# Kernel tuning notes

Hardware: AMD Instinct MI355X
Metric: run time of the kernel (lower is better)

## Reference

```python
import jax, jax.numpy as jnp
import numpy as np

B, H, S_AX, NH, STEPS = 64, 1024, 16384, 8, 16
DH = H // NH
SCALE = 1.0 / np.sqrt(DH)


def setup_inputs():
    key = jax.random.key(0)
    ks = jax.random.split(key, 16)
    s = 0.02
    w = lambda k, shp: jax.random.normal(k, shp, jnp.float32) * s
    return {
        'conjecture': jax.random.normal(ks[0], (B, H), jnp.float32),
        'axiom_emb': jax.random.normal(ks[1], (S_AX, H), jnp.float32),
        'ax_in_w': w(ks[2], (3 * H, H)), 'ax_in_b': jnp.zeros((3 * H,), jnp.float32),
        'ax_out_w': w(ks[3], (H, H)), 'ax_out_b': jnp.zeros((H,), jnp.float32),
        'st_in_w': w(ks[4], (3 * H, H)), 'st_in_b': jnp.zeros((3 * H,), jnp.float32),
        'st_out_w': w(ks[5], (H, H)), 'st_out_b': jnp.zeros((H,), jnp.float32),
        'gen_w1': w(ks[6], (2 * H, 3 * H)), 'gen_b1': jnp.zeros((2 * H,), jnp.float32),
        'ln_g': jnp.ones((2 * H,), jnp.float32), 'ln_b': jnp.zeros((2 * H,), jnp.float32),
        'gen_w2': w(ks[7], (H, 2 * H)), 'gen_b2': jnp.zeros((H,), jnp.float32),
        'val_w1': w(ks[8], (H, H)), 'val_b1': jnp.zeros((H,), jnp.float32),
        'val_w2': w(ks[9], (1, H)), 'val_b2': jnp.zeros((1,), jnp.float32),
        'wih0': w(ks[10], (4 * H, H)), 'whh0': w(ks[11], (4 * H, H)),
        'bih0': jnp.zeros((4 * H,), jnp.float32), 'bhh0': jnp.zeros((4 * H,), jnp.float32),
        'wih1': w(ks[12], (4 * H, H)), 'whh1': w(ks[13], (4 * H, H)),
        'bih1': jnp.zeros((4 * H,), jnp.float32), 'bhh1': jnp.zeros((4 * H,), jnp.float32),
        'max_steps': STEPS,
    }


def _layernorm(x, g, b, eps=1e-5):
    m = x.mean(-1, keepdims=True)
    v = jnp.mean((x - m) ** 2, axis=-1, keepdims=True)
    return (x - m) / jnp.sqrt(v + eps) * g + b


def _lstm_cell(x, h, c, wih, whh, bih, bhh):
    g = x @ wih.T + bih + h @ whh.T + bhh
    i, f, gg, o = jnp.split(g, 4, axis=-1)  # torch gate order: i, f, g, o
    c = jax.nn.sigmoid(f) * c + jax.nn.sigmoid(i) * jnp.tanh(gg)
    return jax.nn.sigmoid(o) * jnp.tanh(c), c


def _validity(x, w1, b1, w2, b2):
    return jax.nn.sigmoid(jax.nn.gelu(x @ w1.T + b1, approximate=False) @ w2.T + b2)


def _forward(conjecture, axiom_emb, ax_in_w, ax_in_b, ax_out_w, ax_out_b,
             st_in_w, st_in_b, st_out_w, st_out_b,
             gen_w1, gen_b1, ln_g, ln_b, gen_w2, gen_b2,
             val_w1, val_b1, val_w2, val_b2,
             wih0, whh0, bih0, bhh0, wih1, whh1, bih1, bhh1, max_steps):
    Bc = conjecture.shape[0]
    Wq_a, Wk_a, Wv_a = jnp.split(ax_in_w, 3, 0)
    bq_a, bk_a, bv_a = jnp.split(ax_in_b, 3, 0)
    Wq_s, Wk_s, Wv_s = jnp.split(st_in_w, 3, 0)
    bq_s, bk_s, bv_s = jnp.split(st_in_b, 3, 0)
    # axiom embeddings are constant across steps/batch -> project K/V once
    kp_a = (axiom_emb @ Wk_a.T + bk_a).reshape(-1, NH, DH)  # [S_ax, nh, dh]
    vp_a = (axiom_emb @ Wv_a.T + bv_a).reshape(-1, NH, DH)
    state = conjecture
    steps = [state]
    h0 = jnp.zeros((Bc, H), state.dtype)
    c0 = jnp.zeros((Bc, H), state.dtype)
    h1 = jnp.zeros((Bc, H), state.dtype)
    c1 = jnp.zeros((Bc, H), state.dtype)
    for _ in range(max_steps):
        # axiom attention (q_len=1, keys shared across batch)
        qa = ((state @ Wq_a.T + bq_a).reshape(Bc, NH, DH)) * SCALE
        attn_a = jax.nn.softmax(jnp.einsum('bnd,snd->bns', qa, kp_a), axis=-1)
        ax_out = jnp.einsum('bns,snd->bnd', attn_a, vp_a).reshape(Bc, H) @ ax_out_w.T + ax_out_b
        # step attention over growing proof memory [T, B, H]
        mem = jnp.stack(steps, 0)
        T = mem.shape[0]
        qs = ((state @ Wq_s.T + bq_s).reshape(Bc, NH, DH)) * SCALE
        kp_s = (mem @ Wk_s.T + bk_s).reshape(T, Bc, NH, DH)
        vp_s = (mem @ Wv_s.T + bv_s).reshape(T, Bc, NH, DH)
        attn_s = jax.nn.softmax(jnp.einsum('bnd,tbnd->bnt', qs, kp_s), axis=-1)
        st_out = jnp.einsum('bnt,tbnd->bnd', attn_s, vp_s).reshape(Bc, H) @ st_out_w.T + st_out_b
        # 2-layer LSTM memory (output unused by the source forward, state carried)
        h0, c0 = _lstm_cell(state, h0, c0, wih0, whh0, bih0, bhh0)
        h1, c1 = _lstm_cell(h0, h1, c1, wih1, whh1, bih1, bhh1)
        # concat -> Linear -> LayerNorm -> GELU -> Linear
        comb = jnp.concatenate([state, ax_out, st_out], axis=-1)
        x = jax.nn.gelu(_layernorm(comb @ gen_w1.T + gen_b1, ln_g, ln_b), approximate=False)
        state = x @ gen_w2.T + gen_b2
        steps.append(state)
    val = _validity(state, val_w1, val_b1, val_w2, val_b2)
    return jnp.stack(steps, 0), val


def reference(conjecture, axiom_emb, ax_in_w, ax_in_b, ax_out_w, ax_out_b,
              st_in_w, st_in_b, st_out_w, st_out_b,
              gen_w1, gen_b1, ln_g, ln_b, gen_w2, gen_b2,
              val_w1, val_b1, val_w2, val_b2,
              wih0, whh0, bih0, bhh0, wih1, whh1, bih1, bhh1, max_steps):
    return _forward(conjecture, axiom_emb, ax_in_w, ax_in_b, ax_out_w, ax_out_b,
                    st_in_w, st_in_b, st_out_w, st_out_b,
                    gen_w1, gen_b1, ln_g, ln_b, gen_w2, gen_b2,
                    val_w1, val_b1, val_w2, val_b2,
                    wih0, whh0, bih0, bhh0, wih1, whh1, bih1, bhh1, max_steps)
```

## Files before the change

kernel.cpp:

```cpp
#include <hip/hip_runtime.h>
#include <stdint.h>


typedef __attribute__((ext_vector_type(8))) short  bfx8;
typedef __attribute__((ext_vector_type(4))) float  f32x4;

#define MFMA16(a, b, c) __builtin_amdgcn_mfma_f32_16x16x32_bf16((a), (b), (c), 0, 0, 0)

#define SCALE_QK 0.08838834764831845f

__device__ __forceinline__ unsigned short f2bf(float f) {
  union { float f; unsigned int u; } v; v.f = f;
  unsigned int r = (v.u + 0x7FFFu + ((v.u >> 16) & 1u)) >> 16;
  return (unsigned short)r;
}

__device__ __forceinline__ float gelu_exact(float x) {
  return 0.5f * x * (1.0f + erff(x * 0.70710678118654752f));
}

__device__ __forceinline__ bfx8 ld8(const unsigned short* p) {
  return *reinterpret_cast<const bfx8*>(p);
}

struct CvtAll {
  const float* s[7];
  unsigned short* d[7];
  int n4[7];
};

__global__ __launch_bounds__(256) void cvt_all_k(CvtAll c) {
  int reg = blockIdx.y;
  const float* s = c.s[reg];
  unsigned short* d = c.d[reg];
  int n4 = c.n4[reg];
  int stride = gridDim.x * 256;
  for (int i = blockIdx.x * 256 + threadIdx.x; i < n4; i += stride) {
    float4 v = reinterpret_cast<const float4*>(s)[i];
    ushort4 o;
    o.x = f2bf(v.x); o.y = f2bf(v.y); o.z = f2bf(v.z); o.w = f2bf(v.w);
    reinterpret_cast<ushort4*>(d)[i] = o;
  }
}

__global__ __launch_bounds__(256) void init_state_k(const float* __restrict__ conj,
                                                    float* __restrict__ out0,
                                                    unsigned short* __restrict__ comb) {
  int i = blockIdx.x * 256 + threadIdx.x;
  float v = conj[i];
  out0[i] = v;
  int b = i >> 10, c = i & 1023;
  comb[b * 3072 + c] = f2bf(v);
}

__global__ __launch_bounds__(256) void kvproj_k(const float* __restrict__ aemb,
                                                const unsigned short* __restrict__ Wkv,
                                                const float* __restrict__ bias,
                                                unsigned short* __restrict__ kp,
                                                unsigned short* __restrict__ vpT) {
  __shared__ __align__(16) unsigned short Asl[128 * 40];
  __shared__ __align__(16) unsigned short Bsl[128 * 40];
  int m0 = blockIdx.x * 128, n0 = blockIdx.y * 128;
  int tid = threadIdx.x;
  int w = tid >> 6, l = tid & 63;
  int wm = w >> 1, wn = w & 1;
  int lane16 = l & 15, kg = l >> 4;
  int srow = tid >> 1, shalf = tid & 1;

  const float* Ag = aemb + (size_t)(m0 + srow) * 1024 + shalf * 16;
  const unsigned short* Bg = Wkv + (size_t)(n0 + srow) * 1024 + shalf * 16;
  unsigned short* As = &Asl[srow * 40 + shalf * 16];
  unsigned short* Bs = &Bsl[srow * 40 + shalf * 16];

  f32x4 acc[4][4];
  f32x4 zz = {0.f, 0.f, 0.f, 0.f};
#pragma unroll
  for (int a = 0; a < 4; a++)
#pragma unroll
    for (int b = 0; b < 4; b++) acc[a][b] = zz;

  for (int k0 = 0; k0 < 1024; k0 += 32) {
    float4 f0 = *(const float4*)(Ag + k0);
    float4 f1 = *(const float4*)(Ag + k0 + 4);
    float4 f2 = *(const float4*)(Ag + k0 + 8);
    float4 f3 = *(const float4*)(Ag + k0 + 12);
    ushort4 u0, u1, u2, u3;
    u0.x = f2bf(f0.x); u0.y = f2bf(f0.y); u0.z = f2bf(f0.z); u0.w = f2bf(f0.w);
    u1.x = f2bf(f1.x); u1.y = f2bf(f1.y); u1.z = f2bf(f1.z); u1.w = f2bf(f1.w);
    u2.x = f2bf(f2.x); u2.y = f2bf(f2.y); u2.z = f2bf(f2.z); u2.w = f2bf(f2.w);
    u3.x = f2bf(f3.x); u3.y = f2bf(f3.y); u3.z = f2bf(f3.z); u3.w = f2bf(f3.w);
    bfx8 b0 = ld8(Bg + k0);
    bfx8 b1 = ld8(Bg + k0 + 8);

    __syncthreads();
    *(ushort4*)(As + 0) = u0;
    *(ushort4*)(As + 4) = u1;
    *(ushort4*)(As + 8) = u2;
    *(ushort4*)(As + 12) = u3;
    *reinterpret_cast<bfx8*>(Bs) = b0;
    *reinterpret_cast<bfx8*>(Bs + 8) = b1;
    __syncthreads();

    bfx8 af[4], bfr[4];
#pragma unroll
    for (int mr = 0; mr < 4; mr++)
      af[mr] = *reinterpret_cast<const bfx8*>(&Asl[(wm * 64 + mr * 16 + lane16) * 40 + kg * 8]);
#pragma unroll
    for (int nr = 0; nr < 4; nr++)
      bfr[nr] = *reinterpret_cast<const bfx8*>(&Bsl[(wn * 64 + nr * 16 + lane16) * 40 + kg * 8]);
#pragma unroll
    for (int mr = 0; mr < 4; mr++)
#pragma unroll
      for (int nr = 0; nr < 4; nr++)
        acc[mr][nr] = MFMA16(af[mr], bfr[nr], acc[mr][nr]);
  }

#pragma unroll
  for (int mr = 0; mr < 4; mr++)
#pragma unroll
    for (int nr = 0; nr < 4; nr++) {
      int rowg0 = m0 + wm * 64 + mr * 16 + kg * 4;
      int colg = n0 + wn * 64 + nr * 16 + lane16;
      float bi = bias[colg];
#pragma unroll
      for (int r = 0; r < 4; r++) {
        float v = acc[mr][nr][r] + bi;
        unsigned short bv = f2bf(v);
        int rg = rowg0 + r;
        if (colg < 1024) kp[(size_t)rg * 1024 + colg] = bv;
        else             vpT[(size_t)(colg - 1024) * 16384 + rg] = bv;
      }
    }
}

struct GemmP {
  const unsigned short* A; int lda;
  const unsigned short* W; int ldw;
  const float* bias;
  int K;
  int epi;
  float scale;
  unsigned short* out_bf; int ldo;
  float* out_f32; int ldo_f;
  float* qs; float* kc; float* vc;
};
struct GemmPair { GemmP pa, pb; int split; };

__global__ __launch_bounds__(256) void gemm64s_k(GemmPair pp) {
  bool first = ((int)blockIdx.x < pp.split);
  GemmP p = first ? pp.pa : pp.pb;
  int ct = first ? blockIdx.x : (blockIdx.x - pp.split);

  int w = threadIdx.x >> 6, l = threadIdx.x & 63;
  int lane16 = l & 15, kg = l >> 4;
  int col = ct * 16 + lane16;
  int kq = p.K >> 2;
  int lda = p.lda;
  const unsigned short* Wb = p.W + (size_t)col * p.ldw + w * kq + kg * 8;
  const unsigned short* Ab = p.A + (size_t)lane16 * lda + w * kq + kg * 8;

  f32x4 zz = {0.f, 0.f, 0.f, 0.f};
  f32x4 acc0 = zz, acc1 = zz, acc2 = zz, acc3 = zz;
#pragma unroll 4
  for (int k = 0; k < kq; k += 32) {
    bfx8 bw = ld8(Wb + k);
    acc0 = MFMA16(ld8(Ab + k), bw, acc0);
    acc1 = MFMA16(ld8(Ab + 16 * lda + k), bw, acc1);
    acc2 = MFMA16(ld8(Ab + 32 * lda + k), bw, acc2);
    acc3 = MFMA16(ld8(Ab + 48 * lda + k), bw, acc3);
  }

  __shared__ f32x4 red[16][64];
  red[w * 4 + 0][l] = acc0;
  red[w * 4 + 1][l] = acc1;
  red[w * 4 + 2][l] = acc2;
  red[w * 4 + 3][l] = acc3;
  __syncthreads();
  f32x4 fin = red[0 * 4 + w][l];
  fin += red[1 * 4 + w][l];
  fin += red[2 * 4 + w][l];
  fin += red[3 * 4 + w][l];

  float bi = p.bias[col];
#pragma unroll
  for (int r = 0; r < 4; ++r) {
    int row = w * 16 + kg * 4 + r;
    float v = fin[r] + bi;
    switch (p.epi) {
      case 0:
        p.out_bf[(size_t)row * p.ldo + col] = f2bf(v * p.scale);
        break;
      case 1:
        if (col < 1024)       p.qs[row * 1024 + col] = v;
        else if (col < 2048)  p.kc[row * 1024 + col - 1024] = v;
        else                  p.vc[row * 1024 + col - 2048] = v;
        break;
      case 2:
        p.out_bf[(size_t)row * p.ldo + col] = f2bf(v);
        break;
      case 3:
        p.out_f32[(size_t)row * p.ldo_f + col] = gelu_exact(v);
        break;
      case 4:
        p.out_f32[(size_t)row * p.ldo_f + col] = v;
        break;
      case 5:
        p.out_f32[(size_t)row * p.ldo_f + col] = v;
        p.out_bf[(size_t)row * p.ldo + col] = f2bf(v);
        break;
    }
  }
}

__global__ __launch_bounds__(256) void flash1_k(const unsigned short* __restrict__ qa,
                                                const unsigned short* __restrict__ kp,
                                                const unsigned short* __restrict__ vpT,
                                                float* __restrict__ Opart,
                                                float* __restrict__ mlpart) {
  int head = blockIdx.x >> 5;
  int chunk = blockIdx.x & 31;
  int w = threadIdx.x >> 6, l = threadIdx.x & 63;
  int lane16 = l & 15, kg = l >> 4;

  __shared__ __align__(16) unsigned short P_lds[64 * 72];
  __shared__ float alpha_lds[64];

  bfx8 qf[4];
  {
    const unsigned short* qb = qa + (size_t)(16 * w + lane16) * 1024 + head * 128 + kg * 8;
#pragma unroll
    for (int kk = 0; kk < 4; kk++) qf[kk] = ld8(qb + kk * 32);
  }
  float m_run[4], l_run[4];
#pragma unroll
  for (int r = 0; r < 4; r++) { m_run[r] = -__builtin_inff(); l_run[r] = 0.f; }
  f32x4 zz = {0.f, 0.f, 0.f, 0.f};
  f32x4 Oac[4][2];
#pragma unroll
  for (int mt = 0; mt < 4; mt++) { Oac[mt][0] = zz; Oac[mt][1] = zz; }

  for (int kb = 0; kb < 8; ++kb) {
    int key0 = chunk * 512 + kb * 64;
    f32x4 sa[4] = {zz, zz, zz, zz};
#pragma unroll
    for (int kt = 0; kt < 4; kt++) {
      const unsigned short* kbp = kp + (size_t)(key0 + kt * 16 + lane16) * 1024 + head * 128 + kg * 8;
#pragma unroll
      for (int kk = 0; kk < 4; kk++) sa[kt] = MFMA16(qf[kk], ld8(kbp + kk * 32), sa[kt]);
    }
    __syncthreads();
#pragma unroll
    for (int r = 0; r < 4; r++) {
      float mx = fmaxf(fmaxf(sa[0][r], sa[1][r]), fmaxf(sa[2][r], sa[3][r]));
#pragma unroll
      for (int m = 1; m < 16; m <<= 1) mx = fmaxf(mx, __shfl_xor(mx, m, 64));
      float mnew = fmaxf(m_run[r], mx);
      float al = expf(m_run[r] - mnew);
      int row = 16 * w + kg * 4 + r;
      float rs = 0.f;
#pragma unroll
      for (int kt = 0; kt < 4; kt++) {
        float pv = expf(sa[kt][r] - mnew);
        rs += pv;
        P_lds[row * 72 + kt * 16 + lane16] = f2bf(pv);
      }
#pragma unroll
      for (int m = 1; m < 16; m <<= 1) rs += __shfl_xor(rs, m, 64);
      l_run[r] = l_run[r] * al + rs;
      m_run[r] = mnew;
      if (lane16 == 0) alpha_lds[row] = al;
    }
    __syncthreads();
#pragma unroll
    for (int mt = 0; mt < 4; mt++)
#pragma unroll
      for (int r = 0; r < 4; r++) {
        float al = alpha_lds[mt * 16 + kg * 4 + r];
        Oac[mt][0][r] *= al;
        Oac[mt][1][r] *= al;
      }
    int d0 = w * 32;
#pragma unroll
    for (int ks = 0; ks < 2; ks++) {
      bfx8 pf[4];
#pragma unroll
      for (int mt = 0; mt < 4; mt++)
        pf[mt] = *reinterpret_cast<const bfx8*>(&P_lds[(mt * 16 + lane16) * 72 + ks * 32 + kg * 8]);
#pragma unroll
      for (int dt = 0; dt < 2; dt++) {
        int d = d0 + dt * 16 + lane16;
        bfx8 vf = ld8(vpT + (size_t)(head * 128 + d) * 16384 + key0 + ks * 32 + kg * 8);
#pragma unroll
        for (int mt = 0; mt < 4; mt++) Oac[mt][dt] = MFMA16(pf[mt], vf, Oac[mt][dt]);
      }
    }
  }
  float* mlb = mlpart + (size_t)(head * 32 + chunk) * 128;
  if (lane16 == 0) {
#pragma unroll
    for (int r = 0; r < 4; r++) {
      int row = 16 * w + kg * 4 + r;
      mlb[row] = m_run[r];
      mlb[64 + row] = l_run[r];
    }
  }
  float* Ob = Opart + (size_t)(head * 32 + chunk) * 64 * 128;
#pragma unroll
  for (int mt = 0; mt < 4; mt++)
#pragma unroll
    for (int dt = 0; dt < 2; dt++)
#pragma unroll
      for (int r = 0; r < 4; r++) {
        int row = mt * 16 + kg * 4 + r;
        int d = w * 32 + dt * 16 + lane16;
        Ob[(size_t)row * 128 + d] = Oac[mt][dt][r];
      }
}

__global__ __launch_bounds__(128) void flash2_k(const float* __restrict__ Opart,
                                                const float* __restrict__ mlpart,
                                                unsigned short* __restrict__ axpre) {
  int b = blockIdx.x >> 3, n = blockIdx.x & 7;
  int d = threadIdx.x;
  float mg = -__builtin_inff();
  for (int c = 0; c < 32; ++c) mg = fmaxf(mg, mlpart[(size_t)(n * 32 + c) * 128 + b]);
  float acc = 0.f, lg = 0.f;
  for (int c = 0; c < 32; ++c) {
    const float* mlb = mlpart + (size_t)(n * 32 + c) * 128;
    float sw = expf(mlb[b] - mg);
    lg += mlb[64 + b] * sw;
    acc += sw * Opart[((size_t)(n * 32 + c) * 64 + b) * 128 + d];
  }
  axpre[b * 1024 + n * 128 + d] = f2bf(acc / lg);
}

__global__ __launch_bounds__(128) void stattn_k(const float* __restrict__ qs,
                                                const float* __restrict__ kc,
                                                const float* __restrict__ vc,
                                                unsigned short* __restrict__ stpre,
                                                int T) {
  int b = blockIdx.x >> 3, n = blockIdx.x & 7;
  int tid = threadIdx.x;
  __shared__ float sc[17];
  __shared__ float wred[2];
  int idx = b * 1024 + n * 128 + tid;
  float q = qs[idx] * SCALE_QK;
  for (int t = 0; t < T; ++t) {
    float v = q * kc[t * 65536 + idx];
#pragma unroll
    for (int m = 1; m < 64; m <<= 1) v += __shfl_xor(v, m, 64);
    __syncthreads();
    if ((tid & 63) == 0) wred[tid >> 6] = v;
    __syncthreads();
    if (tid == 0) sc[t] = wred[0] + wred[1];
  }
  __syncthreads();
  float mx = -__builtin_inff();
  for (int t = 0; t < T; ++t) mx = fmaxf(mx, sc[t]);
  float den = 0.f, o = 0.f;
  for (int t = 0; t < T; ++t) {
    float e = expf(sc[t] - mx);
    den += e;
    o += e * vc[t * 65536 + idx];
  }
  stpre[idx] = f2bf(o / den);
}

__global__ __launch_bounds__(256) void ln_gelu_k(const float* __restrict__ g1,
                                                 const float* __restrict__ gam,
                                                 const float* __restrict__ bet,
                                                 unsigned short* __restrict__ xo) {
  int b = blockIdx.x;
  int tid = threadIdx.x;
  __shared__ float red[4];
  const float* row = g1 + b * 2048;
  float s = 0.f;
  for (int i = tid; i < 2048; i += 256) s += row[i];
#pragma unroll
  for (int m = 1; m < 64; m <<= 1) s += __shfl_xor(s, m, 64);
  if ((tid & 63) == 0) red[tid >> 6] = s;
  __syncthreads();
  float mean = (red[0] + red[1] + red[2] + red[3]) * (1.f / 2048.f);
  __syncthreads();
  float v = 0.f;
  for (int i = tid; i < 2048; i += 256) { float d = row[i] - mean; v += d * d; }
#pragma unroll
  for (int m = 1; m < 64; m <<= 1) v += __shfl_xor(v, m, 64);
  if ((tid & 63) == 0) red[tid >> 6] = v;
  __syncthreads();
  float var = (red[0] + red[1] + red[2] + red[3]) * (1.f / 2048.f);
  float inv = 1.0f / sqrtf(var + 1e-5f);
  for (int i = tid; i < 2048; i += 256) {
    float y = (row[i] - mean) * inv * gam[i] + bet[i];
    xo[b * 2048 + i] = f2bf(gelu_exact(y));
  }
}

__global__ __launch_bounds__(64) void val2_k(const float* __restrict__ v1,
                                             const float* __restrict__ w2,
                                             const float* __restrict__ b2,
                                             float* __restrict__ out) {
  int b = blockIdx.x, l = threadIdx.x;
  float s = 0.f;
  for (int k = l; k < 1024; k += 64) s += v1[b * 1024 + k] * w2[k];
#pragma unroll
  for (int m = 1; m < 64; m <<= 1) s += __shfl_xor(s, m, 64);
  if (l == 0) out[b] = 1.f / (1.f + expf(-(s + b2[0])));
}

extern "C" void kernel_launch(void* const* d_in, const int* in_sizes, int n_in,
                              void* d_out, int out_size, void* d_ws, size_t ws_size,
                              hipStream_t stream) {
  (void)in_sizes; (void)n_in; (void)out_size; (void)ws_size;

  const float* conj   = (const float*)d_in[0];
  const float* aemb   = (const float*)d_in[1];
  const float* ax_in_b = (const float*)d_in[3];
  const float* ax_out_b = (const float*)d_in[5];
  const float* st_in_b = (const float*)d_in[7];
  const float* st_out_b = (const float*)d_in[9];
  const float* gen_b1 = (const float*)d_in[11];
  const float* ln_g   = (const float*)d_in[12];
  const float* ln_b   = (const float*)d_in[13];
  const float* gen_b2 = (const float*)d_in[15];
  const float* val_b1 = (const float*)d_in[17];
  const float* val_w2 = (const float*)d_in[18];
  const float* val_b2 = (const float*)d_in[19];

  size_t off = 0;
  char* wsb = (char*)d_ws;
  auto carve = [&](size_t bytes) -> void* {
    void* p = wsb + off;
    off += (bytes + 1023) & ~(size_t)1023;
    return p;
  };
  unsigned short* axw  = (unsigned short*)carve((size_t)3072 * 1024 * 2);
  unsigned short* stw  = (unsigned short*)carve((size_t)3072 * 1024 * 2);
  unsigned short* axow = (unsigned short*)carve((size_t)1024 * 1024 * 2);
  unsigned short* stow = (unsigned short*)carve((size_t)1024 * 1024 * 2);
  unsigned short* g1w  = (unsigned short*)carve((size_t)2048 * 3072 * 2);
  unsigned short* g2w  = (unsigned short*)carve((size_t)1024 * 2048 * 2);
  unsigned short* v1w  = (unsigned short*)carve((size_t)1024 * 1024 * 2);
  unsigned short* kp   = (unsigned short*)carve((size_t)16384 * 1024 * 2);
  unsigned short* vpT  = (unsigned short*)carve((size_t)16384 * 1024 * 2);
  float* kcache = (float*)carve((size_t)16 * 65536 * 4);
  float* vcache = (float*)carve((size_t)16 * 65536 * 4);
  float* Opart  = (float*)carve((size_t)8 * 32 * 64 * 128 * 4);
  float* mlpart = (float*)carve((size_t)8 * 32 * 128 * 4);
  unsigned short* comb = (unsigned short*)carve((size_t)64 * 3072 * 2);
  float* qsb  = (float*)carve((size_t)64 * 1024 * 4);
  unsigned short* qab   = (unsigned short*)carve((size_t)64 * 1024 * 2);
  unsigned short* axpre = (unsigned short*)carve((size_t)64 * 1024 * 2);
  unsigned short* stpre = (unsigned short*)carve((size_t)64 * 1024 * 2);
  float* g1f  = (float*)carve((size_t)64 * 2048 * 4);
  unsigned short* xbf = (unsigned short*)carve((size_t)64 * 2048 * 2);
  float* v1f  = (float*)carve((size_t)64 * 1024 * 4);

  {
    CvtAll c;
    c.s[0] = (const float*)d_in[2];  c.d[0] = axw;  c.n4[0] = 3072 * 1024 / 4;
    c.s[1] = (const float*)d_in[6];  c.d[1] = stw;  c.n4[1] = 3072 * 1024 / 4;
    c.s[2] = (const float*)d_in[4];  c.d[2] = axow; c.n4[2] = 1024 * 1024 / 4;
    c.s[3] = (const float*)d_in[8];  c.d[3] = stow; c.n4[3] = 1024 * 1024 / 4;
    c.s[4] = (const float*)d_in[10]; c.d[4] = g1w;  c.n4[4] = 2048 * 3072 / 4;
    c.s[5] = (const float*)d_in[14]; c.d[5] = g2w;  c.n4[5] = 1024 * 2048 / 4;
    c.s[6] = (const float*)d_in[16]; c.d[6] = v1w;  c.n4[6] = 1024 * 1024 / 4;
    cvt_all_k<<<dim3(512, 7), 256, 0, stream>>>(c);
  }

  float* out_steps = (float*)d_out;
  init_state_k<<<256, 256, 0, stream>>>(conj, out_steps, comb);

  kvproj_k<<<dim3(128, 16), 256, 0, stream>>>(aemb, axw + (size_t)1024 * 1024,
                                              ax_in_b + 1024, kp, vpT);

  auto launch_pair = [&](const GemmP& a, int blka, const GemmP& b, int blkb) {
    GemmPair pp;
    pp.pa = a; pp.pb = b; pp.split = blka;
    gemm64s_k<<<blka + blkb, 256, 0, stream>>>(pp);
  };
  auto launch_one = [&](const GemmP& a, int blka) {
    GemmPair pp;
    pp.pa = a; pp.pb = a; pp.split = blka;
    gemm64s_k<<<blka, 256, 0, stream>>>(pp);
  };

  for (int t = 0; t < 16; ++t) {
    {
      GemmP pa{}, pb{};
      pa.A = comb; pa.lda = 3072; pa.W = axw; pa.ldw = 1024; pa.bias = ax_in_b;
      pa.K = 1024; pa.epi = 0; pa.scale = SCALE_QK; pa.out_bf = qab; pa.ldo = 1024;
      pb.A = comb; pb.lda = 3072; pb.W = stw; pb.ldw = 1024; pb.bias = st_in_b;
      pb.K = 1024; pb.epi = 1;
      pb.qs = qsb; pb.kc = kcache + (size_t)t * 65536; pb.vc = vcache + (size_t)t * 65536;
      launch_pair(pa, 64, pb, 192);
    }
    flash1_k<<<256, 256, 0, stream>>>(qab, kp, vpT, Opart, mlpart);
    flash2_k<<<512, 128, 0, stream>>>(Opart, mlpart, axpre);
    stattn_k<<<512, 128, 0, stream>>>(qsb, kcache, vcache, stpre, t + 1);
    {
      GemmP pa{}, pb{};
      pa.A = axpre; pa.lda = 1024; pa.W = axow; pa.ldw = 1024; pa.bias = ax_out_b;
      pa.K = 1024; pa.epi = 2; pa.out_bf = comb + 1024; pa.ldo = 3072;
      pb.A = stpre; pb.lda = 1024; pb.W = stow; pb.ldw = 1024; pb.bias = st_out_b;
      pb.K = 1024; pb.epi = 2; pb.out_bf = comb + 2048; pb.ldo = 3072;
      launch_pair(pa, 64, pb, 64);
    }
    {
      GemmP p{};
      p.A = comb; p.lda = 3072; p.W = g1w; p.ldw = 3072; p.bias = gen_b1;
      p.K = 3072; p.epi = 4; p.out_f32 = g1f; p.ldo_f = 2048;
      launch_one(p, 128);
    }
    ln_gelu_k<<<64, 256, 0, stream>>>(g1f, ln_g, ln_b, xbf);
    {
      GemmP p{};
      p.A = xbf; p.lda = 2048; p.W = g2w; p.ldw = 2048; p.bias = gen_b2;
      p.K = 2048; p.epi = 5;
      p.out_f32 = out_steps + (size_t)(t + 1) * 65536; p.ldo_f = 1024;
      p.out_bf = comb; p.ldo = 3072;
      launch_one(p, 64);
    }
  }

  {
    GemmP p{};
    p.A = comb; p.lda = 3072; p.W = v1w; p.ldw = 1024; p.bias = val_b1;
    p.K = 1024; p.epi = 3; p.out_f32 = v1f; p.ldo_f = 1024;
    launch_one(p, 64);
  }
  val2_k<<<64, 64, 0, stream>>>(v1f, val_w2, val_b2, out_steps + (size_t)17 * 65536);
}
```

Baseline: 2.051 ms.

## Pre-convert axiom embeddings, split flash into 64 chunks, fuse combine with step attention

The axiom embedding is now converted to bf16 in the bulk conversion kernel, so the K/V projection GEMM loads bf16 directly. That GEMM also gets a swizzled block order and vectorized transposed-V stores. The flash-attention kernel now splits keys into 64 chunks of 256 per head and does a single-pass softmax without the online rescaling, which doubles the grid to 512 blocks. The flash combine and step-attention kernels are merged into one launch. This removes per-tile conversion work and a launch per step, but doubles the partial-output buffers the combine must read.

```diff
diff --git a/kernel.cpp b/kernel.cpp
--- a/kernel.cpp
+++ b/kernel.cpp
@@ -24,9 +24,9 @@
 }
 
 struct CvtAll {
-  const float* s[7];
-  unsigned short* d[7];
-  int n4[7];
+  const float* s[8];
+  unsigned short* d[8];
+  int n4[8];
 };
 
 __global__ __launch_bounds__(256) void cvt_all_k(CvtAll c) {
@@ -53,21 +53,22 @@
   comb[b * 3072 + c] = f2bf(v);
 }
 
-__global__ __launch_bounds__(256) void kvproj_k(const float* __restrict__ aemb,
+__global__ __launch_bounds__(256) void kvproj_k(const unsigned short* __restrict__ aembh,
                                                 const unsigned short* __restrict__ Wkv,
                                                 const float* __restrict__ bias,
                                                 unsigned short* __restrict__ kp,
                                                 unsigned short* __restrict__ vpT) {
   __shared__ __align__(16) unsigned short Asl[128 * 40];
   __shared__ __align__(16) unsigned short Bsl[128 * 40];
-  int m0 = blockIdx.x * 128, n0 = blockIdx.y * 128;
+  int lin = ((int)blockIdx.x & 7) * 256 + ((int)blockIdx.x >> 3);
+  int m0 = (lin >> 4) * 128, n0 = (lin & 15) * 128;
   int tid = threadIdx.x;
   int w = tid >> 6, l = tid & 63;
   int wm = w >> 1, wn = w & 1;
   int lane16 = l & 15, kg = l >> 4;
   int srow = tid >> 1, shalf = tid & 1;
 
-  const float* Ag = aemb + (size_t)(m0 + srow) * 1024 + shalf * 16;
+  const unsigned short* Ag = aembh + (size_t)(m0 + srow) * 1024 + shalf * 16;
   const unsigned short* Bg = Wkv + (size_t)(n0 + srow) * 1024 + shalf * 16;
   unsigned short* As = &Asl[srow * 40 + shalf * 16];
   unsigned short* Bs = &Bsl[srow * 40 + shalf * 16];
@@ -80,23 +81,14 @@
     for (int b = 0; b < 4; b++) acc[a][b] = zz;
 
   for (int k0 = 0; k0 < 1024; k0 += 32) {
-    float4 f0 = *(const float4*)(Ag + k0);
-    float4 f1 = *(const float4*)(Ag + k0 + 4);
-    float4 f2 = *(const float4*)(Ag + k0 + 8);
-    float4 f3 = *(const float4*)(Ag + k0 + 12);
-    ushort4 u0, u1, u2, u3;
-    u0.x = f2bf(f0.x); u0.y = f2bf(f0.y); u0.z = f2bf(f0.z); u0.w = f2bf(f0.w);
-    u1.x = f2bf(f1.x); u1.y = f2bf(f1.y); u1.z = f2bf(f1.z); u1.w = f2bf(f1.w);
-    u2.x = f2bf(f2.x); u2.y = f2bf(f2.y); u2.z = f2bf(f2.z); u2.w = f2bf(f2.w);
-    u3.x = f2bf(f3.x); u3.y = f2bf(f3.y); u3.z = f2bf(f3.z); u3.w = f2bf(f3.w);
+    bfx8 a0 = ld8(Ag + k0);
+    bfx8 a1 = ld8(Ag + k0 + 8);
     bfx8 b0 = ld8(Bg + k0);
     bfx8 b1 = ld8(Bg + k0 + 8);
 
     __syncthreads();
-    *(ushort4*)(As + 0) = u0;
-    *(ushort4*)(As + 4) = u1;
-    *(ushort4*)(As + 8) = u2;
-    *(ushort4*)(As + 12) = u3;
+    *reinterpret_cast<bfx8*>(As) = a0;
+    *reinterpret_cast<bfx8*>(As + 8) = a1;
     *reinterpret_cast<bfx8*>(Bs) = b0;
     *reinterpret_cast<bfx8*>(Bs + 8) = b1;
     __syncthreads();
@@ -122,13 +114,17 @@
       int rowg0 = m0 + wm * 64 + mr * 16 + kg * 4;
       int colg = n0 + wn * 64 + nr * 16 + lane16;
       float bi = bias[colg];
-#pragma unroll
-      for (int r = 0; r < 4; r++) {
-        float v = acc[mr][nr][r] + bi;
-        unsigned short bv = f2bf(v);
-        int rg = rowg0 + r;
-        if (colg < 1024) kp[(size_t)rg * 1024 + colg] = bv;
-        else             vpT[(size_t)(colg - 1024) * 16384 + rg] = bv;
+      if (colg < 1024) {
+#pragma unroll
+        for (int r = 0; r < 4; r++)
+          kp[(size_t)(rowg0 + r) * 1024 + colg] = f2bf(acc[mr][nr][r] + bi);
+      } else {
+        ushort4 pk;
+        pk.x = f2bf(acc[mr][nr][0] + bi);
+        pk.y = f2bf(acc[mr][nr][1] + bi);
+        pk.z = f2bf(acc[mr][nr][2] + bi);
+        pk.w = f2bf(acc[mr][nr][3] + bi);
+        *reinterpret_cast<ushort4*>(&vpT[(size_t)(colg - 1024) * 16384 + rowg0]) = pk;
       }
     }
 }
@@ -217,13 +213,13 @@
                                                 const unsigned short* __restrict__ vpT,
                                                 float* __restrict__ Opart,
                                                 float* __restrict__ mlpart) {
-  int head = blockIdx.x >> 5;
-  int chunk = blockIdx.x & 31;
+  int head = blockIdx.x >> 6;
+  int chunk = blockIdx.x & 63;
+  int key0 = chunk * 256;
   int w = threadIdx.x >> 6, l = threadIdx.x & 63;
   int lane16 = l & 15, kg = l >> 4;
 
-  __shared__ __align__(16) unsigned short P_lds[64 * 72];
-  __shared__ float alpha_lds[64];
+  __shared__ __align__(16) unsigned short P_lds[64 * 264];
 
   bfx8 qf[4];
   {
@@ -231,139 +227,127 @@
 #pragma unroll
     for (int kk = 0; kk < 4; kk++) qf[kk] = ld8(qb + kk * 32);
   }
-  float m_run[4], l_run[4];
-#pragma unroll
-  for (int r = 0; r < 4; r++) { m_run[r] = -__builtin_inff(); l_run[r] = 0.f; }
+
   f32x4 zz = {0.f, 0.f, 0.f, 0.f};
+  f32x4 sa[16];
+#pragma unroll
+  for (int kt = 0; kt < 16; kt++) {
+    const unsigned short* kbp = kp + (size_t)(key0 + kt * 16 + lane16) * 1024 + head * 128 + kg * 8;
+    f32x4 s = zz;
+#pragma unroll
+    for (int kk = 0; kk < 4; kk++) s = MFMA16(qf[kk], ld8(kbp + kk * 32), s);
+    sa[kt] = s;
+  }
+
+  float mrow[4], lrow[4];
+#pragma unroll
+  for (int r = 0; r < 4; r++) {
+    float mx = sa[0][r];
+#pragma unroll
+    for (int kt = 1; kt < 16; kt++) mx = fmaxf(mx, sa[kt][r]);
+#pragma unroll
+    for (int m = 1; m < 16; m <<= 1) mx = fmaxf(mx, __shfl_xor(mx, m, 64));
+    int row = 16 * w + kg * 4 + r;
+    float rs = 0.f;
+#pragma unroll
+    for (int kt = 0; kt < 16; kt++) {
+      float pv = expf(sa[kt][r] - mx);
+      rs += pv;
+      P_lds[row * 264 + kt * 16 + lane16] = f2bf(pv);
+    }
+#pragma unroll
+    for (int m = 1; m < 16; m <<= 1) rs += __shfl_xor(rs, m, 64);
+    mrow[r] = mx;
+    lrow[r] = rs;
+  }
+  __syncthreads();
+
   f32x4 Oac[4][2];
 #pragma unroll
   for (int mt = 0; mt < 4; mt++) { Oac[mt][0] = zz; Oac[mt][1] = zz; }
-
-  for (int kb = 0; kb < 8; ++kb) {
-    int key0 = chunk * 512 + kb * 64;
-    f32x4 sa[4] = {zz, zz, zz, zz};
-#pragma unroll
-    for (int kt = 0; kt < 4; kt++) {
-      const unsigned short* kbp = kp + (size_t)(key0 + kt * 16 + lane16) * 1024 + head * 128 + kg * 8;
-#pragma unroll
-      for (int kk = 0; kk < 4; kk++) sa[kt] = MFMA16(qf[kk], ld8(kbp + kk * 32), sa[kt]);
-    }
-    __syncthreads();
-#pragma unroll
-    for (int r = 0; r < 4; r++) {
-      float mx = fmaxf(fmaxf(sa[0][r], sa[1][r]), fmaxf(sa[2][r], sa[3][r]));
-#pragma unroll
-      for (int m = 1; m < 16; m <<= 1) mx = fmaxf(mx, __shfl_xor(mx, m, 64));
-      float mnew = fmaxf(m_run[r], mx);
-      float al = expf(m_run[r] - mnew);
-      int row = 16 * w + kg * 4 + r;
-      float rs = 0.f;
-#pragma unroll
-      for (int kt = 0; kt < 4; kt++) {
-        float pv = expf(sa[kt][r] - mnew);
-        rs += pv;
-        P_lds[row * 72 + kt * 16 + lane16] = f2bf(pv);
-      }
-#pragma unroll
-      for (int m = 1; m < 16; m <<= 1) rs += __shfl_xor(rs, m, 64);
-      l_run[r] = l_run[r] * al + rs;
-      m_run[r] = mnew;
-      if (lane16 == 0) alpha_lds[row] = al;
-    }
-    __syncthreads();
+#pragma unroll
+  for (int ks = 0; ks < 8; ks++) {
+    bfx8 pf[4];
 #pragma unroll
     for (int mt = 0; mt < 4; mt++)
-#pragma unroll
-      for (int r = 0; r < 4; r++) {
-        float al = alpha_lds[mt * 16 + kg * 4 + r];
-        Oac[mt][0][r] *= al;
-        Oac[mt][1][r] *= al;
-      }
-    int d0 = w * 32;
-#pragma unroll
-    for (int ks = 0; ks < 2; ks++) {
-      bfx8 pf[4];
-#pragma unroll
-      for (int mt = 0; mt < 4; mt++)
-        pf[mt] = *reinterpret_cast<const bfx8*>(&P_lds[(mt * 16 + lane16) * 72 + ks * 32 + kg * 8]);
-#pragma unroll
-      for (int dt = 0; dt < 2; dt++) {
-        int d = d0 + dt * 16 + lane16;
-        bfx8 vf = ld8(vpT + (size_t)(head * 128 + d) * 16384 + key0 + ks * 32 + kg * 8);
-#pragma unroll
-        for (int mt = 0; mt < 4; mt++) Oac[mt][dt] = MFMA16(pf[mt], vf, Oac[mt][dt]);
-      }
-    }
-  }
-  float* mlb = mlpart + (size_t)(head * 32 + chunk) * 128;
+      pf[mt] = *reinterpret_cast<const bfx8*>(&P_lds[(mt * 16 + lane16) * 264 + ks * 32 + kg * 8]);
+#pragma unroll
+    for (int dt = 0; dt < 2; dt++) {
+      int d = w * 32 + dt * 16 + lane16;
+      bfx8 vf = ld8(vpT + (size_t)(head * 128 + d) * 16384 + key0 + ks * 32 + kg * 8);
+#pragma unroll
+      for (int mt = 0; mt < 4; mt++) Oac[mt][dt] = MFMA16(pf[mt], vf, Oac[mt][dt]);
+    }
+  }
+
+  float* mlb = mlpart + (size_t)(head * 64 + chunk) * 128;
   if (lane16 == 0) {
 #pragma unroll
     for (int r = 0; r < 4; r++) {
       int row = 16 * w + kg * 4 + r;
-      mlb[row] = m_run[r];
-      mlb[64 + row] = l_run[r];
-    }
-  }
-  float* Ob = Opart + (size_t)(head * 32 + chunk) * 64 * 128;
+      mlb[row] = mrow[r];
+      mlb[64 + row] = lrow[r];
+    }
+  }
+  float* Ob = Opart + (size_t)(head * 64 + chunk) * 64 * 128;
 #pragma unroll
   for (int mt = 0; mt < 4; mt++)
 #pragma unroll
     for (int dt = 0; dt < 2; dt++)
 #pragma unroll
-      for (int r = 0; r < 4; r++) {
-        int row = mt * 16 + kg * 4 + r;
-        int d = w * 32 + dt * 16 + lane16;
-        Ob[(size_t)row * 128 + d] = Oac[mt][dt][r];
-      }
-}
-
-__global__ __launch_bounds__(128) void flash2_k(const float* __restrict__ Opart,
-                                                const float* __restrict__ mlpart,
-                                                unsigned short* __restrict__ axpre) {
-  int b = blockIdx.x >> 3, n = blockIdx.x & 7;
-  int d = threadIdx.x;
-  float mg = -__builtin_inff();
-  for (int c = 0; c < 32; ++c) mg = fmaxf(mg, mlpart[(size_t)(n * 32 + c) * 128 + b]);
-  float acc = 0.f, lg = 0.f;
-  for (int c = 0; c < 32; ++c) {
-    const float* mlb = mlpart + (size_t)(n * 32 + c) * 128;
-    float sw = expf(mlb[b] - mg);
-    lg += mlb[64 + b] * sw;
-    acc += sw * Opart[((size_t)(n * 32 + c) * 64 + b) * 128 + d];
-  }
-  axpre[b * 1024 + n * 128 + d] = f2bf(acc / lg);
-}
-
-__global__ __launch_bounds__(128) void stattn_k(const float* __restrict__ qs,
-                                                const float* __restrict__ kc,
-                                                const float* __restrict__ vc,
-                                                unsigned short* __restrict__ stpre,
-                                                int T) {
-  int b = blockIdx.x >> 3, n = blockIdx.x & 7;
-  int tid = threadIdx.x;
-  __shared__ float sc[17];
-  __shared__ float wred[2];
-  int idx = b * 1024 + n * 128 + tid;
-  float q = qs[idx] * SCALE_QK;
-  for (int t = 0; t < T; ++t) {
-    float v = q * kc[t * 65536 + idx];
-#pragma unroll
-    for (int m = 1; m < 64; m <<= 1) v += __shfl_xor(v, m, 64);
+      for (int r = 0; r < 4; r++)
+        Ob[(size_t)(mt * 16 + kg * 4 + r) * 128 + w * 32 + dt * 16 + lane16] = Oac[mt][dt][r];
+}
+
+__global__ __launch_bounds__(128) void f2st_k(const float* __restrict__ Opart,
+                                              const float* __restrict__ mlpart,
+                                              unsigned short* __restrict__ axpre,
+                                              const float* __restrict__ qs,
+                                              const float* __restrict__ kc,
+                                              const float* __restrict__ vc,
+                                              unsigned short* __restrict__ stpre,
+                                              int T) {
+  if ((int)blockIdx.x < 512) {
+    int b = blockIdx.x >> 3, n = blockIdx.x & 7;
+    int d = threadIdx.x;
+    float mg = -__builtin_inff();
+    for (int c = 0; c < 64; ++c) mg = fmaxf(mg, mlpart[(size_t)(n * 64 + c) * 128 + b]);
+    float acc = 0.f, lg = 0.f;
+    for (int c = 0; c < 64; ++c) {
+      const float* mlb = mlpart + (size_t)(n * 64 + c) * 128;
+      float sw = expf(mlb[b] - mg);
+      lg += mlb[64 + b] * sw;
+      acc += sw * Opart[((size_t)(n * 64 + c) * 64 + b) * 128 + d];
+    }
+    axpre[b * 1024 + n * 128 + d] = f2bf(acc / lg);
+  } else {
+    int bi = blockIdx.x - 512;
+    int b = bi >> 3, n = bi & 7;
+    int tid = threadIdx.x;
+    __shared__ float sc[17];
+    __shared__ float wred[2];
+    int idx = b * 1024 + n * 128 + tid;
+    float q = qs[idx] * SCALE_QK;
+    for (int t = 0; t < T; ++t) {
+      float v = q * kc[t * 65536 + idx];
+#pragma unroll
+      for (int m = 1; m < 64; m <<= 1) v += __shfl_xor(v, m, 64);
+      __syncthreads();
+      if ((tid & 63) == 0) wred[tid >> 6] = v;
+      __syncthreads();
+      if (tid == 0) sc[t] = wred[0] + wred[1];
+    }
     __syncthreads();
-    if ((tid & 63) == 0) wred[tid >> 6] = v;
-    __syncthreads();
-    if (tid == 0) sc[t] = wred[0] + wred[1];
-  }
-  __syncthreads();
-  float mx = -__builtin_inff();
-  for (int t = 0; t < T; ++t) mx = fmaxf(mx, sc[t]);
-  float den = 0.f, o = 0.f;
-  for (int t = 0; t < T; ++t) {
-    float e = expf(sc[t] - mx);
-    den += e;
-    o += e * vc[t * 65536 + idx];
-  }
-  stpre[idx] = f2bf(o / den);
+    float mx = -__builtin_inff();
+    for (int t = 0; t < T; ++t) mx = fmaxf(mx, sc[t]);
+    float den = 0.f, o = 0.f;
+    for (int t = 0; t < T; ++t) {
+      float e = expf(sc[t] - mx);
+      den += e;
+      o += e * vc[t * 65536 + idx];
+    }
+    stpre[idx] = f2bf(o / den);
+  }
 }
 
 __global__ __launch_bounds__(256) void ln_gelu_k(const float* __restrict__ g1,
@@ -441,12 +425,13 @@
   unsigned short* g1w  = (unsigned short*)carve((size_t)2048 * 3072 * 2);
   unsigned short* g2w  = (unsigned short*)carve((size_t)1024 * 2048 * 2);
   unsigned short* v1w  = (unsigned short*)carve((size_t)1024 * 1024 * 2);
+  unsigned short* aembh = (unsigned short*)carve((size_t)16384 * 1024 * 2);
   unsigned short* kp   = (unsigned short*)carve((size_t)16384 * 1024 * 2);
   unsigned short* vpT  = (unsigned short*)carve((size_t)16384 * 1024 * 2);
   float* kcache = (float*)carve((size_t)16 * 65536 * 4);
   float* vcache = (float*)carve((size_t)16 * 65536 * 4);
-  float* Opart  = (float*)carve((size_t)8 * 32 * 64 * 128 * 4);
-  float* mlpart = (float*)carve((size_t)8 * 32 * 128 * 4);
+  float* Opart  = (float*)carve((size_t)8 * 64 * 64 * 128 * 4);
+  float* mlpart = (float*)carve((size_t)8 * 64 * 128 * 4);
   unsigned short* comb = (unsigned short*)carve((size_t)64 * 3072 * 2);
   float* qsb  = (float*)carve((size_t)64 * 1024 * 4);
   unsigned short* qab   = (unsigned short*)carve((size_t)64 * 1024 * 2);
@@ -458,21 +443,22 @@
 
   {
     CvtAll c;
-    c.s[0] = (const float*)d_in[2];  c.d[0] = axw;  c.n4[0] = 3072 * 1024 / 4;
-    c.s[1] = (const float*)d_in[6];  c.d[1] = stw;  c.n4[1] = 3072 * 1024 / 4;
-    c.s[2] = (const float*)d_in[4];  c.d[2] = axow; c.n4[2] = 1024 * 1024 / 4;
-    c.s[3] = (const float*)d_in[8];  c.d[3] = stow; c.n4[3] = 1024 * 1024 / 4;
-    c.s[4] = (const float*)d_in[10]; c.d[4] = g1w;  c.n4[4] = 2048 * 3072 / 4;
-    c.s[5] = (const float*)d_in[14]; c.d[5] = g2w;  c.n4[5] = 1024 * 2048 / 4;
-    c.s[6] = (const float*)d_in[16]; c.d[6] = v1w;  c.n4[6] = 1024 * 1024 / 4;
-    cvt_all_k<<<dim3(512, 7), 256, 0, stream>>>(c);
+    c.s[0] = (const float*)d_in[2];  c.d[0] = axw;   c.n4[0] = 3072 * 1024 / 4;
+    c.s[1] = (const float*)d_in[6];  c.d[1] = stw;   c.n4[1] = 3072 * 1024 / 4;
+    c.s[2] = (const float*)d_in[4];  c.d[2] = axow;  c.n4[2] = 1024 * 1024 / 4;
+    c.s[3] = (const float*)d_in[8];  c.d[3] = stow;  c.n4[3] = 1024 * 1024 / 4;
+    c.s[4] = (const float*)d_in[10]; c.d[4] = g1w;   c.n4[4] = 2048 * 3072 / 4;
+    c.s[5] = (const float*)d_in[14]; c.d[5] = g2w;   c.n4[5] = 1024 * 2048 / 4;
+    c.s[6] = (const float*)d_in[16]; c.d[6] = v1w;   c.n4[6] = 1024 * 1024 / 4;
+    c.s[7] = aemb;                   c.d[7] = aembh; c.n4[7] = 16384 * 1024 / 4;
+    cvt_all_k<<<dim3(512, 8), 256, 0, stream>>>(c);
   }
 
   float* out_steps = (float*)d_out;
   init_state_k<<<256, 256, 0, stream>>>(conj, out_steps, comb);
 
-  kvproj_k<<<dim3(128, 16), 256, 0, stream>>>(aemb, axw + (size_t)1024 * 1024,
-                                              ax_in_b + 1024, kp, vpT);
+  kvproj_k<<<2048, 256, 0, stream>>>(aembh, axw + (size_t)1024 * 1024,
+                                     ax_in_b + 1024, kp, vpT);
 
   auto launch_pair = [&](const GemmP& a, int blka, const GemmP& b, int blkb) {
     GemmPair pp;
@@ -495,9 +481,9 @@
       pb.qs = qsb; pb.kc = kcache + (size_t)t * 65536; pb.vc = vcache + (size_t)t * 65536;
       launch_pair(pa, 64, pb, 192);
     }
-    flash1_k<<<256, 256, 0, stream>>>(qab, kp, vpT, Opart, mlpart);
-    flash2_k<<<512, 128, 0, stream>>>(Opart, mlpart, axpre);
-    stattn_k<<<512, 128, 0, stream>>>(qsb, kcache, vcache, stpre, t + 1);
+    flash1_k<<<512, 256, 0, stream>>>(qab, kp, vpT, Opart, mlpart);
+    f2st_k<<<1024, 128, 0, stream>>>(Opart, mlpart, axpre, qsb, kcache, vcache,
+                                     stpre, t + 1);
     {
       GemmP pa{}, pb{};
       pa.A = axpre; pa.lda = 1024; pa.W = axow; pa.ldw = 1024; pa.bias = ax_out_b;
```

Result: faster. 1.931 ms (-5.8%).
